# Optimization experiments

Measured on AMD Instinct MI355X. Metric: run time of the kernel, lower is better.

The kernel has to match this reference:

```python
import jax, jax.numpy as jnp
import numpy as np

N = 100000   # nodes
E = 1600000  # edges
H = 64       # hidden_dim
NT = 512     # num_taxo
TD = 32      # taxo_dim
ID = 32      # item_dim
L = 2        # taxo_layers
ETA = 0.5
SLOPE = 0.01  # leaky_relu default


def setup_inputs() -> dict:
    key = jax.random.key(0)
    ks = jax.random.split(key, 20)
    p = lambda i, shape, s: jax.random.normal(ks[i], shape, dtype=jnp.float32) * s
    return {
        'h': p(0, (N, H), 1.0),
        'src': jax.random.randint(ks[1], (E,), 0, N),
        'dst': jax.random.randint(ks[2], (E,), 0, N),
        'taxo_cats': jax.random.randint(ks[3], (N, L), 0, NT),
        'idx_rows': jnp.arange(N),
        'idx_cols': jax.random.randint(ks[4], (N,), 0, N),
        'idx_vals': jax.random.uniform(ks[5], (N,), dtype=jnp.float32),
        'norm_rows': jnp.arange(N),
        'norm_cols': jax.random.randint(ks[6], (N,), 0, N),
        'norm_vals': jax.random.uniform(ks[7], (N,), dtype=jnp.float32),
        'W_w': p(8, (H, H), H ** -0.5),
        'W_b': jnp.zeros((H,), jnp.float32),
        'prelu_a': jnp.full((1,), 0.25, jnp.float32),
        'taxo_mean': p(9, (NT, H), 0.1),
        'taxo_std_log': p(10, (NT, H), 0.1),
        'conv_wh': p(11, (1, 2 * H), (2 * H) ** -0.5),
        'conv_Ww': p(12, (H, H), H ** -0.5),
        'conv_Wb': jnp.zeros((H,), jnp.float32),
        'psi_W': p(13, (1, H, H), H ** -0.5),
        'psi_b': jnp.zeros((1,), jnp.float32),
        'mlp_w0': p(14, (TD, H), H ** -0.5),
        'mlp_b0': jnp.zeros((TD,), jnp.float32),
        'mlp_w1': p(15, (TD, H), H ** -0.5),
        'mlp_b1': jnp.zeros((TD,), jnp.float32),
        'mlp_w2': p(16, (ID, H), H ** -0.5),
        'mlp_b2': jnp.zeros((ID,), jnp.float32),
    }


def _spmm(rows, cols, vals, x, nrows):
    # sparse COO [nrows, n] @ dense [n, d]
    return jax.ops.segment_sum(vals[:, None] * x[cols], rows, num_segments=nrows)


def _edge_softmax(scores, dst, n):
    # softmax of edge scores grouped by destination node
    m = jax.ops.segment_max(scores, dst, num_segments=n)
    e = jnp.exp(scores - m[dst])
    s = jax.ops.segment_sum(e, dst, num_segments=n)
    return e / s[dst]


def _prelu(x, a):
    return jnp.where(x >= 0, x, a * x)


def _normalize(x):
    return x / jnp.maximum(jnp.linalg.norm(x, axis=1, keepdims=True), 1e-12)


def _conv(h, tax, src, dst, wh, Ww, Wb):
    hs = h[src]  # [E,H]
    wf = jnp.concatenate([hs, h[dst]], axis=1) @ wh.T  # [E,1]
    wf = jnp.where(wf >= 0, wf, SLOPE * wf)
    alpha_f = _edge_softmax(wf, dst, N)
    wt = jnp.sum(tax[src] * tax[dst], axis=1, keepdims=True)  # [E,1]
    alpha_t = _edge_softmax(wt, dst, N)
    alpha = ETA * alpha_f + (1.0 - ETA) * alpha_t
    z = jax.ops.segment_sum(hs * alpha, dst, num_segments=N)  # u_mul_e + sum
    return z @ Ww.T + Wb


def reference(h, src, dst, taxo_cats, idx_rows, idx_cols, idx_vals,
              norm_rows, norm_cols, norm_vals, W_w, W_b, prelu_a,
              taxo_mean, taxo_std_log, conv_wh, conv_Ww, conv_Wb,
              psi_W, psi_b, mlp_w0, mlp_b0, mlp_w1, mlp_b1, mlp_w2, mlp_b2):
    h = _prelu(h @ W_w.T + W_b, prelu_a)
    means = taxo_mean[taxo_cats]            # [N,L,H]
    stds = jnp.exp(taxo_std_log[taxo_cats])  # [N,L,H]
    tax = _spmm(norm_rows, norm_cols, norm_vals, means.reshape(N, L * H), N)
    # conv layers share the SAME weights (ModuleList([ConvLayer]*num_layer))
    for i in range(2):
        h = _conv(h, tax, src, dst, conv_wh, conv_Ww, conv_Wb)
        if i < 1:
            h = _prelu(h, prelu_a)
    raw = h
    emb_h = _normalize(h @ mlp_w2.T + mlp_b2)
    embs = []
    for i, (w, b) in enumerate([(mlp_w0, mlp_b0), (mlp_w1, mlp_b1)]):
        h_rev = _spmm(idx_rows, idx_cols, idx_vals, h, N)
        mi = means[:, i]
        si = stds[:, i]
        stpl = jnp.einsum('bi,ij,bj->b', h_rev, psi_W[0], mi)[:, None] + psi_b
        tau = jax.nn.sigmoid(stpl) * jnp.exp(-si)
        cur = (1.0 - tau) * h_rev + tau * mi
        cur = _spmm(norm_rows, norm_cols, norm_vals, cur, N)
        embs.append(_normalize(cur @ w.T + b))
    emb = jnp.stack(embs, axis=2).reshape(N, -1)
    emb = jnp.concatenate([emb_h, emb], axis=1)  # [N, out_dim]
    return raw, emb
```

## Files before the change

### kernel.cpp

```cpp
#include <hip/hip_runtime.h>

constexpr int H  = 64;
constexpr int NT = 512;
constexpr int NBMAX = 512;

#define FMA4(acc_, s_, v_) { (acc_).x += (s_)*(v_).x; (acc_).y += (s_)*(v_).y; \
                             (acc_).z += (s_)*(v_).z; (acc_).w += (s_)*(v_).w; }

__global__ void k_gram(const float* __restrict__ tm, float* __restrict__ G) {
    int idx = blockIdx.x * blockDim.x + threadIdx.x;
    if (idx >= NT * NT) return;
    int a = idx >> 9, b = idx & (NT - 1);
    const float* ra = tm + a * H;
    const float* rb = tm + b * H;
    float s = 0.f;
#pragma unroll
    for (int k = 0; k < H; ++k) s += ra[k] * rb[k];
    G[idx] = s;
}

__global__ void k_nm(const int* __restrict__ ncols, const int* __restrict__ cats,
                     const float* __restrict__ nvals, uint2* __restrict__ nm, int N) {
    int n = blockIdx.x * blockDim.x + threadIdx.x;
    if (n >= N) return;
    int j = ncols[n];
    nm[n] = make_uint2(__float_as_uint(nvals[n]),
                       (unsigned)(cats[j * 2] | (cats[j * 2 + 1] << 16)));
}

__global__ void k_phist(const int* __restrict__ dst, int* __restrict__ histT,
                        int NB, int NPB, int CH, int E) {
    __shared__ int hist[NBMAX];
    int b = blockIdx.x, t = threadIdx.x;
    for (int i = t; i < NB; i += 256) hist[i] = 0;
    __syncthreads();
    int e0 = b * CH, e1 = min(E, e0 + CH);
    for (int e = e0 + t; e < e1; e += 256)
        atomicAdd(&hist[dst[e] >> 8], 1);
    __syncthreads();
    for (int i = t; i < NB; i += 256) histT[i * NPB + b] = hist[i];
}

__global__ void k_btot(const int* __restrict__ histT, int* __restrict__ tot, int NPB) {
    __shared__ int sh[256];
    int bk = blockIdx.x, t = threadIdx.x;
    int s = 0;
    for (int j = t; j < NPB; j += 256) s += histT[bk * NPB + j];
    sh[t] = s;
    __syncthreads();
    for (int o = 128; o; o >>= 1) { if (t < o) sh[t] += sh[t + o]; __syncthreads(); }
    if (!t) tot[bk] = sh[0];
}

__global__ void k_bscan(const int* __restrict__ tot, int* __restrict__ bbase,
                        int* __restrict__ row_start, int NB, int N, int E) {
    __shared__ int sh[NBMAX];
    int t = threadIdx.x;
    int v = (t < NB) ? tot[t] : 0;
    sh[t] = v;
    __syncthreads();
    for (int o = 1; o < NBMAX; o <<= 1) {
        int x = (t >= o) ? sh[t - o] : 0;
        __syncthreads();
        sh[t] += x;
        __syncthreads();
    }
    if (t < NB) bbase[t] = sh[t] - v;
    if (t == 0) { bbase[NB] = E; row_start[N] = E; }
}

__global__ void k_boff(const int* __restrict__ histT, const int* __restrict__ bbase,
                       int* __restrict__ boff, int NPB) {
    __shared__ int sh[NBMAX];
    int bk = blockIdx.x, t = threadIdx.x;
    int v = (t < NPB) ? histT[bk * NPB + t] : 0;
    sh[t] = v;
    __syncthreads();
    for (int o = 1; o < NBMAX; o <<= 1) {
        int x = (t >= o) ? sh[t - o] : 0;
        __syncthreads();
        sh[t] += x;
        __syncthreads();
    }
    if (t < NPB) boff[bk * NPB + t] = bbase[bk] + sh[t] - v;
}

__global__ void k_part(const int* __restrict__ src, const int* __restrict__ dst,
                       const int* __restrict__ boff, unsigned* __restrict__ brec,
                       int NB, int NPB, int CH, int E) {
    __shared__ int cur[NBMAX];
    int b = blockIdx.x, t = threadIdx.x;
    for (int i = t; i < NB; i += 256) cur[i] = boff[i * NPB + b];
    __syncthreads();
    int e0 = b * CH, e1 = min(E, e0 + CH);
    for (int e = e0 + t; e < e1; e += 256) {
        int s = src[e], d = dst[e];
        int pos = atomicAdd(&cur[d >> 8], 1);
        brec[pos] = (unsigned)s | ((unsigned)(d & 255) << 24);
    }
}

__global__ void k_csr(const unsigned* __restrict__ brec, const int* __restrict__ bbase,
                      const uint2* __restrict__ nm, const float* __restrict__ G,
                      int* __restrict__ row_start, int* __restrict__ src_s,
                      float* __restrict__ et, float* __restrict__ sumt, int N) {
    __shared__ int   sdeg[256];
    __shared__ int   scur[256];
    __shared__ float ssum[256];
    __shared__ float snv[256];
    __shared__ int   scc[256];
    int b = blockIdx.x, t = threadIdx.x;
    int node0 = b << 8;
    int ebase = bbase[b], eend = bbase[b + 1];
    sdeg[t] = 0; scur[t] = 0; ssum[t] = 0.f;
    int n = node0 + t;
    if (n < N) { uint2 m = nm[n]; snv[t] = __uint_as_float(m.x); scc[t] = (int)m.y; }
    __syncthreads();
    for (int i = ebase + t; i < eend; i += 256)
        atomicAdd(&sdeg[brec[i] >> 24], 1);
    __syncthreads();
    int val = sdeg[t];
    for (int o = 1; o < 256; o <<= 1) {
        int x = (t >= o) ? sdeg[t - o] : 0;
        __syncthreads();
        sdeg[t] += x;
        __syncthreads();
    }
    int gstart = ebase + sdeg[t] - val;
    if (n < N) row_start[n] = gstart;
    sdeg[t] = gstart;
    __syncthreads();
    for (int i = ebase + t; i < eend; i += 256) {
        unsigned r = brec[i];
        int s = (int)(r & 0xFFFFFFu);
        int j = (int)(r >> 24);
        int c = atomicAdd(&scur[j], 1);
        int k = sdeg[j] + c;
        src_s[k] = s;
        uint2 ms = nm[s];
        float nvs = __uint_as_float(ms.x);
        int cs = (int)ms.y;
        int cd = scc[j];
        float wt = nvs * snv[j] *
                   (G[(cs & 0xffff) * NT + (cd & 0xffff)] + G[(cs >> 16) * NT + (cd >> 16)]);
        float ev = __expf(wt);
        et[k] = ev;
        atomicAdd(&ssum[j], ev);
    }
    __syncthreads();
    if (n < N) sumt[n] = ssum[t];
}

__global__ void k_agg(const float* __restrict__ h_in, const int* __restrict__ src_s,
                      const int* __restrict__ row_start, const float* __restrict__ et,
                      const float* __restrict__ sumt, const float* __restrict__ s_u,
                      const float* __restrict__ s_v, float* __restrict__ z_out, int N) {
    int t = threadIdx.x;
    int sg = t >> 4, l16 = t & 15, f = l16 * 4;
    int n = blockIdx.x * 16 + sg;
    if (n >= N) return;
    int kb = row_start[n], ke = row_start[n + 1];
    float4 z = make_float4(0.f, 0.f, 0.f, 0.f);
    if (ke > kb) {
        float sv = s_v[n];
        float invt = 0.5f / sumt[n];
        float ssf = 0.f;
        float4 zf0 = z, zf1 = z, zt0 = z, zt1 = z;
        for (int k0 = kb; k0 < ke; k0 += 16) {
            int cnt = ke - k0; cnt = cnt < 16 ? cnt : 16;
            int cl = cnt - 1;
            int myk = k0 + (l16 <= cl ? l16 : cl);
            int ms = src_s[myk];
            float me = et[myk] * invt;
            float mw = s_u[ms] + sv;
            mw = mw >= 0.f ? mw : 0.01f * mw;
            float mf = __expf(mw);
            if (l16 > cl) { mf = 0.f; me = 0.f; }
            ssf += mf;
            for (int j0 = 0; j0 < cnt; j0 += 4) {
                int jB = min(j0 + 1, cl), jC = min(j0 + 2, cl), jD = min(j0 + 3, cl);
                int sA = __shfl(ms, j0, 16), sB = __shfl(ms, jB, 16);
                int sC = __shfl(ms, jC, 16), sD = __shfl(ms, jD, 16);
                float tfA = __shfl(mf, j0, 16), tfB = __shfl(mf, jB, 16);
                float tfC = __shfl(mf, jC, 16), tfD = __shfl(mf, jD, 16);
                float teA = __shfl(me, j0, 16), teB = __shfl(me, jB, 16);
                float teC = __shfl(me, jC, 16), teD = __shfl(me, jD, 16);
                float fB = (j0 + 1 <= cl) ? tfB : 0.f;
                float fC = (j0 + 2 <= cl) ? tfC : 0.f;
                float fD = (j0 + 3 <= cl) ? tfD : 0.f;
                float eB = (j0 + 1 <= cl) ? teB : 0.f;
                float eC = (j0 + 2 <= cl) ? teC : 0.f;
                float eD = (j0 + 3 <= cl) ? teD : 0.f;
                const float4 hA = *reinterpret_cast<const float4*>(h_in + (size_t)sA * H + f);
                const float4 hB = *reinterpret_cast<const float4*>(h_in + (size_t)sB * H + f);
                const float4 hC = *reinterpret_cast<const float4*>(h_in + (size_t)sC * H + f);
                const float4 hD = *reinterpret_cast<const float4*>(h_in + (size_t)sD * H + f);
                FMA4(zf0, tfA, hA); FMA4(zt0, teA, hA);
                FMA4(zf1, fB, hB);  FMA4(zt1, eB, hB);
                FMA4(zf0, fC, hC);  FMA4(zt0, eC, hC);
                FMA4(zf1, fD, hD);  FMA4(zt1, eD, hD);
            }
        }
        ssf += __shfl_xor(ssf, 1); ssf += __shfl_xor(ssf, 2);
        ssf += __shfl_xor(ssf, 4); ssf += __shfl_xor(ssf, 8);
        float invf = 0.5f / ssf;
        z.x = (zf0.x + zf1.x) * invf + (zt0.x + zt1.x);
        z.y = (zf0.y + zf1.y) * invf + (zt0.y + zt1.y);
        z.z = (zf0.z + zf1.z) * invf + (zt0.z + zt1.z);
        z.w = (zf0.w + zf1.w) * invf + (zt0.w + zt1.w);
    }
    *reinterpret_cast<float4*>(z_out + (size_t)n * H + f) = z;
}

template <bool PRELU, bool SUV, bool EMBH>
__global__ void __launch_bounds__(256, 4)
k_trans(const float* __restrict__ in, const float* __restrict__ W,
        const float* __restrict__ b, const float* __restrict__ a_ptr,
        const float* __restrict__ wh,
        float* __restrict__ s_u_o, float* __restrict__ s_v_o,
        const float* __restrict__ w2, const float* __restrict__ b2,
        float* __restrict__ emb_out,
        float* __restrict__ out, int N) {
    __shared__ float WF[64 * 68];
    __shared__ float W2T[EMBH ? 64 * 36 : 1];
    __shared__ float xs[4][8][68];
    int t = threadIdx.x;
    for (int i = t; i < 64 * 64; i += 256) { int j = i >> 6, l = i & 63; WF[l * 68 + j] = W[i]; }
    if constexpr (EMBH) {
        for (int i = t; i < 64 * 32; i += 256) { int j = i >> 6, l = i & 63; W2T[l * 36 + j] = w2[i]; }
    }
    __syncthreads();
    int wid = t >> 6, lane = t & 63;
    int g = lane >> 4, f = lane & 15;
    float a = PRELU ? a_ptr[0] : 0.f;
    float4 bias = *reinterpret_cast<const float4*>(b + 4 * f);
    int n0 = blockIdx.x * 32 + wid * 8 + g;
    int n1 = n0 + 4;
    float4 xv0 = make_float4(0.f, 0.f, 0.f, 0.f), xv1 = xv0;
    if (n0 < N) xv0 = *reinterpret_cast<const float4*>(in + (size_t)n0 * H + 4 * f);
    if (n1 < N) xv1 = *reinterpret_cast<const float4*>(in + (size_t)n1 * H + 4 * f);
    *reinterpret_cast<float4*>(&xs[wid][g][4 * f])     = xv0;
    *reinterpret_cast<float4*>(&xs[wid][4 + g][4 * f]) = xv1;
    float4 accP = make_float4(0.f, 0.f, 0.f, 0.f), accQ = accP;
#pragma unroll 2
    for (int l0 = 0; l0 < 64; l0 += 4) {
        const float* wp = &WF[l0 * 68 + 4 * f];
        float4 wv0 = *reinterpret_cast<const float4*>(wp);
        float4 wv1 = *reinterpret_cast<const float4*>(wp + 68);
        float4 wv2 = *reinterpret_cast<const float4*>(wp + 136);
        float4 wv3 = *reinterpret_cast<const float4*>(wp + 204);
        float4 xP = *reinterpret_cast<const float4*>(&xs[wid][g][l0]);
        float4 xQ = *reinterpret_cast<const float4*>(&xs[wid][4 + g][l0]);
        FMA4(accP, xP.x, wv0); FMA4(accP, xP.y, wv1);
        FMA4(accP, xP.z, wv2); FMA4(accP, xP.w, wv3);
        FMA4(accQ, xQ.x, wv0); FMA4(accQ, xQ.y, wv1);
        FMA4(accQ, xQ.z, wv2); FMA4(accQ, xQ.w, wv3);
    }
    auto epi = [&](float4 acc, int n, int slot) {
        acc.x += bias.x; acc.y += bias.y; acc.z += bias.z; acc.w += bias.w;
        if constexpr (PRELU) {
            acc.x = acc.x >= 0.f ? acc.x : a * acc.x;
            acc.y = acc.y >= 0.f ? acc.y : a * acc.y;
            acc.z = acc.z >= 0.f ? acc.z : a * acc.z;
            acc.w = acc.w >= 0.f ? acc.w : a * acc.w;
        }
        if (n < N) *reinterpret_cast<float4*>(out + (size_t)n * H + 4 * f) = acc;
        if constexpr (SUV) {
            float4 wu = *reinterpret_cast<const float4*>(wh + 4 * f);
            float4 wv = *reinterpret_cast<const float4*>(wh + H + 4 * f);
            float u = acc.x * wu.x + acc.y * wu.y + acc.z * wu.z + acc.w * wu.w;
            float v = acc.x * wv.x + acc.y * wv.y + acc.z * wv.z + acc.w * wv.w;
            u += __shfl_xor(u, 1); v += __shfl_xor(v, 1);
            u += __shfl_xor(u, 2); v += __shfl_xor(v, 2);
            u += __shfl_xor(u, 4); v += __shfl_xor(v, 4);
            u += __shfl_xor(u, 8); v += __shfl_xor(v, 8);
            if (f == 0 && n < N) { s_u_o[n] = u; s_v_o[n] = v; }
        }
        if constexpr (EMBH) {
            *reinterpret_cast<float4*>(&xs[wid][slot][4 * f]) = acc;
            if (f < 8) {
                float4 e4 = *reinterpret_cast<const float4*>(b2 + 4 * f);
#pragma unroll 4
                for (int l0 = 0; l0 < 64; l0 += 4) {
                    float4 x4 = *reinterpret_cast<const float4*>(&xs[wid][slot][l0]);
                    float4 u0 = *reinterpret_cast<const float4*>(&W2T[(l0 + 0) * 36 + 4 * f]);
                    float4 u1 = *reinterpret_cast<const float4*>(&W2T[(l0 + 1) * 36 + 4 * f]);
                    float4 u2 = *reinterpret_cast<const float4*>(&W2T[(l0 + 2) * 36 + 4 * f]);
                    float4 u3 = *reinterpret_cast<const float4*>(&W2T[(l0 + 3) * 36 + 4 * f]);
                    FMA4(e4, x4.x, u0); FMA4(e4, x4.y, u1);
                    FMA4(e4, x4.z, u2); FMA4(e4, x4.w, u3);
                }
                float sq = e4.x * e4.x + e4.y * e4.y + e4.z * e4.z + e4.w * e4.w;
                sq += __shfl_xor(sq, 1);
                sq += __shfl_xor(sq, 2);
                sq += __shfl_xor(sq, 4);
                float invn = 1.f / fmaxf(sqrtf(sq), 1e-12f);
                e4.x *= invn; e4.y *= invn; e4.z *= invn; e4.w *= invn;
                if (n < N) *reinterpret_cast<float4*>(emb_out + (size_t)n * 96 + 4 * f) = e4;
            }
        }
    };
    epi(accP, n0, g);
    epi(accQ, n1, 4 + g);
}

__global__ void __launch_bounds__(256, 4)
k_post1(const float* __restrict__ raw, const int* __restrict__ icols,
        const float* __restrict__ ivals, const float* __restrict__ Psi,
        const float* __restrict__ psib, const int* __restrict__ cats,
        const float* __restrict__ tm, const float* __restrict__ tsl,
        float* __restrict__ cur0, float* __restrict__ cur1, int N) {
    __shared__ float PF[64 * 68];
    __shared__ float xs[4][8][68];
    int t = threadIdx.x;
    for (int i = t; i < 64 * 64; i += 256) { int l = i >> 6, j = i & 63; PF[l * 68 + j] = Psi[i]; }
    __syncthreads();
    int wid = t >> 6, lane = t & 63;
    int g = lane >> 4, f = lane & 15;
    float pb = psib[0];
    int n0 = blockIdx.x * 32 + wid * 8 + g;
    int n1 = n0 + 4;
    float4 hr0 = make_float4(0.f, 0.f, 0.f, 0.f), hr1 = hr0;
    if (n0 < N) {
        int c = icols[n0]; float iv = ivals[n0];
        float4 rv = *reinterpret_cast<const float4*>(raw + (size_t)c * H + 4 * f);
        hr0.x = iv * rv.x; hr0.y = iv * rv.y; hr0.z = iv * rv.z; hr0.w = iv * rv.w;
    }
    if (n1 < N) {
        int c = icols[n1]; float iv = ivals[n1];
        float4 rv = *reinterpret_cast<const float4*>(raw + (size_t)c * H + 4 * f);
        hr1.x = iv * rv.x; hr1.y = iv * rv.y; hr1.z = iv * rv.z; hr1.w = iv * rv.w;
    }
    *reinterpret_cast<float4*>(&xs[wid][g][4 * f])     = hr0;
    *reinterpret_cast<float4*>(&xs[wid][4 + g][4 * f]) = hr1;
    float4 v0 = make_float4(0.f, 0.f, 0.f, 0.f), v1 = v0;
#pragma unroll 2
    for (int l0 = 0; l0 < 64; l0 += 4) {
        const float* pp = &PF[l0 * 68 + 4 * f];
        float4 pv0 = *reinterpret_cast<const float4*>(pp);
        float4 pv1 = *reinterpret_cast<const float4*>(pp + 68);
        float4 pv2 = *reinterpret_cast<const float4*>(pp + 136);
        float4 pv3 = *reinterpret_cast<const float4*>(pp + 204);
        float4 xP = *reinterpret_cast<const float4*>(&xs[wid][g][l0]);
        float4 xQ = *reinterpret_cast<const float4*>(&xs[wid][4 + g][l0]);
        FMA4(v0, xP.x, pv0); FMA4(v0, xP.y, pv1); FMA4(v0, xP.z, pv2); FMA4(v0, xP.w, pv3);
        FMA4(v1, xQ.x, pv0); FMA4(v1, xQ.y, pv1); FMA4(v1, xQ.z, pv2); FMA4(v1, xQ.w, pv3);
    }
    auto epi = [&](float4 v, float4 hr, int n) {
        if (n >= N) return;
#pragma unroll
        for (int i2 = 0; i2 < 2; ++i2) {
            int c = cats[n * 2 + i2];
            float4 m4 = *reinterpret_cast<const float4*>(tm + (size_t)c * H + 4 * f);
            float sd = v.x * m4.x + v.y * m4.y + v.z * m4.z + v.w * m4.w;
            sd += __shfl_xor(sd, 1);
            sd += __shfl_xor(sd, 2);
            sd += __shfl_xor(sd, 4);
            sd += __shfl_xor(sd, 8);
            float sig = 1.f / (1.f + __expf(-(sd + pb)));
            float4 t4 = *reinterpret_cast<const float4*>(tsl + (size_t)c * H + 4 * f);
            float4 tau, cv;
            tau.x = sig * __expf(-__expf(t4.x));
            tau.y = sig * __expf(-__expf(t4.y));
            tau.z = sig * __expf(-__expf(t4.z));
            tau.w = sig * __expf(-__expf(t4.w));
            cv.x = (1.f - tau.x) * hr.x + tau.x * m4.x;
            cv.y = (1.f - tau.y) * hr.y + tau.y * m4.y;
            cv.z = (1.f - tau.z) * hr.z + tau.z * m4.z;
            cv.w = (1.f - tau.w) * hr.w + tau.w * m4.w;
            *reinterpret_cast<float4*>((i2 ? cur1 : cur0) + (size_t)n * H + 4 * f) = cv;
        }
    };
    epi(v0, hr0, n0);
    epi(v1, hr1, n1);
}

__global__ void __launch_bounds__(256, 4)
k_post2(const float* __restrict__ cur0, const float* __restrict__ cur1,
        const int* __restrict__ ncols, const float* __restrict__ nvals,
        const float* __restrict__ w0, const float* __restrict__ b0,
        const float* __restrict__ w1, const float* __restrict__ b1,
        float* __restrict__ emb_out, int N) {
    __shared__ float WC[64 * 68];
    __shared__ float xs[4][4][2][68];
    int t = threadIdx.x;
    for (int i = t; i < 64 * 64; i += 256) {
        int j = i >> 6, l = i & 63;
        WC[l * 68 + j] = (j < 32) ? w0[j * 64 + l] : w1[(j - 32) * 64 + l];
    }
    __syncthreads();
    int wid = t >> 6, lane = t & 63;
    int g = lane >> 4, f = lane & 15;
    int half = f >> 3;
    const float* bb = half ? b1 : b0;
    float4 bias = *reinterpret_cast<const float4*>(bb + 4 * (f & 7));
    for (int it = 0; it < 2; ++it) {
        int n = blockIdx.x * 32 + wid * 8 + it * 4 + g;
        float4 x0 = make_float4(0.f, 0.f, 0.f, 0.f), x1 = x0;
        if (n < N) {
            int c = ncols[n];
            float gsc = nvals[n];
            float4 c0v = *reinterpret_cast<const float4*>(cur0 + (size_t)c * H + 4 * f);
            float4 c1v = *reinterpret_cast<const float4*>(cur1 + (size_t)c * H + 4 * f);
            x0.x = gsc * c0v.x; x0.y = gsc * c0v.y; x0.z = gsc * c0v.z; x0.w = gsc * c0v.w;
            x1.x = gsc * c1v.x; x1.y = gsc * c1v.y; x1.z = gsc * c1v.z; x1.w = gsc * c1v.w;
        }
        *reinterpret_cast<float4*>(&xs[wid][g][0][4 * f]) = x0;
        *reinterpret_cast<float4*>(&xs[wid][g][1][4 * f]) = x1;
        float4 acc = bias;
#pragma unroll 4
        for (int l0 = 0; l0 < 64; l0 += 4) {
            float4 x4  = *reinterpret_cast<const float4*>(&xs[wid][g][half][l0]);
            float4 wv0 = *reinterpret_cast<const float4*>(&WC[(l0 + 0) * 68 + 4 * f]);
            float4 wv1 = *reinterpret_cast<const float4*>(&WC[(l0 + 1) * 68 + 4 * f]);
            float4 wv2 = *reinterpret_cast<const float4*>(&WC[(l0 + 2) * 68 + 4 * f]);
            float4 wv3 = *reinterpret_cast<const float4*>(&WC[(l0 + 3) * 68 + 4 * f]);
            FMA4(acc, x4.x, wv0); FMA4(acc, x4.y, wv1);
            FMA4(acc, x4.z, wv2); FMA4(acc, x4.w, wv3);
        }
        float sq = acc.x * acc.x + acc.y * acc.y + acc.z * acc.z + acc.w * acc.w;
        sq += __shfl_xor(sq, 1);
        sq += __shfl_xor(sq, 2);
        sq += __shfl_xor(sq, 4);
        float invn = 1.f / fmaxf(sqrtf(sq), 1e-12f);
        if (n < N) {
            int jb = (f & 7) * 4;
            float* o = emb_out + (size_t)n * 96 + 32 + half;
            o[2 * (jb + 0)] = acc.x * invn;
            o[2 * (jb + 1)] = acc.y * invn;
            o[2 * (jb + 2)] = acc.z * invn;
            o[2 * (jb + 3)] = acc.w * invn;
        }
    }
}

extern "C" void kernel_launch(void* const* d_in, const int* in_sizes, int n_in,
                              void* d_out, int out_size, void* d_ws, size_t ws_size,
                              hipStream_t stream) {
    const float* h      = (const float*)d_in[0];
    const int*   src    = (const int*)d_in[1];
    const int*   dst    = (const int*)d_in[2];
    const int*   cats   = (const int*)d_in[3];
    const int*   icols  = (const int*)d_in[5];
    const float* ivals  = (const float*)d_in[6];
    const int*   ncols  = (const int*)d_in[8];
    const float* nvals  = (const float*)d_in[9];
    const float* W_w    = (const float*)d_in[10];
    const float* W_b    = (const float*)d_in[11];
    const float* pre_a  = (const float*)d_in[12];
    const float* tm     = (const float*)d_in[13];
    const float* tsl    = (const float*)d_in[14];
    const float* wh     = (const float*)d_in[15];
    const float* cWw    = (const float*)d_in[16];
    const float* cWb    = (const float*)d_in[17];
    const float* psiW   = (const float*)d_in[18];
    const float* psib   = (const float*)d_in[19];
    const float* w0     = (const float*)d_in[20];
    const float* b0     = (const float*)d_in[21];
    const float* w1     = (const float*)d_in[22];
    const float* b1     = (const float*)d_in[23];
    const float* w2     = (const float*)d_in[24];
    const float* b2     = (const float*)d_in[25];

    const int N = in_sizes[0] / H;
    const int E = in_sizes[1];
    const int NB = (N + 255) >> 8;
    const int NPB = NB;
    const int CH = (E + NPB - 1) / NPB;

    char* ws = (char*)d_ws;
    size_t off = 0;
    auto alloc = [&](size_t bytes) -> void* {
        void* p = ws + off;
        off = (off + bytes + 255) & ~(size_t)255;
        return p;
    };
    float*    A        = (float*)   alloc((size_t)N * H * 4);
    float*    B        = (float*)   alloc((size_t)N * H * 4);
    float*    Z        = (float*)   alloc((size_t)N * H * 4);
    float*    et       = (float*)   alloc((size_t)E * 4);
    int*      src_s    = (int*)     alloc((size_t)E * 4);
    unsigned* brec     = (unsigned*)alloc((size_t)E * 4);
    uint2*    nm       = (uint2*)   alloc((size_t)N * 8);
    int*      row_start= (int*)     alloc((size_t)(N + 1) * 4);
    float*    sumt     = (float*)   alloc((size_t)N * 4);
    float*    s_u0     = (float*)   alloc((size_t)N * 4);
    float*    s_v0     = (float*)   alloc((size_t)N * 4);
    float*    s_u1     = (float*)   alloc((size_t)N * 4);
    float*    s_v1     = (float*)   alloc((size_t)N * 4);
    float*    G        = (float*)   alloc((size_t)NT * NT * 4);
    int*      histT    = (int*)     alloc((size_t)NB * NPB * 4);
    int*      boff     = (int*)     alloc((size_t)NB * NPB * 4);
    int*      tot      = (int*)     alloc((size_t)NB * 4);
    int*      bbase    = (int*)     alloc((size_t)(NB + 1) * 4);
    (void)ws_size; (void)n_in; (void)out_size;

    float* rawOut  = (float*)d_out;
    float* emb_out = (float*)d_out + (size_t)N * H;

    dim3 b256(256);
    int nb16 = (N + 15) / 16;
    int nb32 = (N + 31) / 32;

    k_gram<<<(NT * NT + 255) / 256, b256, 0, stream>>>(tm, G);
    k_nm<<<(N + 255) / 256, b256, 0, stream>>>(ncols, cats, nvals, nm, N);
    k_phist<<<NPB, b256, 0, stream>>>(dst, histT, NB, NPB, CH, E);
    k_btot<<<NB, b256, 0, stream>>>(histT, tot, NPB);
    k_bscan<<<1, NBMAX, 0, stream>>>(tot, bbase, row_start, NB, N, E);
    k_boff<<<NB, NBMAX, 0, stream>>>(histT, bbase, boff, NPB);
    k_part<<<NPB, b256, 0, stream>>>(src, dst, boff, brec, NB, NPB, CH, E);
    k_csr<<<NB, b256, 0, stream>>>(brec, bbase, nm, G, row_start, src_s, et, sumt, N);

    k_trans<true, true, false><<<nb32, b256, 0, stream>>>(
        h, W_w, W_b, pre_a, wh, s_u0, s_v0, nullptr, nullptr, nullptr, A, N);

    k_agg<<<nb16, b256, 0, stream>>>(A, src_s, row_start, et, sumt, s_u0, s_v0, Z, N);
    k_trans<true, true, false><<<nb32, b256, 0, stream>>>(
        Z, cWw, cWb, pre_a, wh, s_u1, s_v1, nullptr, nullptr, nullptr, B, N);

    k_agg<<<nb16, b256, 0, stream>>>(B, src_s, row_start, et, sumt, s_u1, s_v1, Z, N);
    k_trans<false, false, true><<<nb32, b256, 0, stream>>>(
        Z, cWw, cWb, pre_a, nullptr, nullptr, nullptr, w2, b2, emb_out, rawOut, N);

    k_post1<<<nb32, b256, 0, stream>>>(rawOut, icols, ivals, psiW, psib, cats, tm, tsl,
                                       A, B, N);
    k_post2<<<nb32, b256, 0, stream>>>(A, B, ncols, nvals, w0, b0, w1, b1, emb_out, N);
}
```

Before: 354.8 us.

## Fuse edge aggregation with the dense transform, and fold k_nm into k_phist

Aggregation and the following 64x64 transform (with PReLU, attention-score projection, or the emb_h head) now run in one kernel, k_aggt, via a small per-group staging buffer in shared memory. This removes the round trip of the intermediate Z array through global memory and two kernel launches. Each 16-node block now loads the full weight matrix into shared memory, which adds per-block setup and shared-memory pressure. The node-metadata pack (k_nm) is merged into the histogram kernel, which assumes the histogram grid has at least N/256 blocks.

```diff
diff --git a/kernel.cpp b/kernel.cpp
--- a/kernel.cpp
+++ b/kernel.cpp
@@ -19,19 +19,18 @@
     G[idx] = s;
 }
 
-__global__ void k_nm(const int* __restrict__ ncols, const int* __restrict__ cats,
-                     const float* __restrict__ nvals, uint2* __restrict__ nm, int N) {
-    int n = blockIdx.x * blockDim.x + threadIdx.x;
-    if (n >= N) return;
-    int j = ncols[n];
-    nm[n] = make_uint2(__float_as_uint(nvals[n]),
-                       (unsigned)(cats[j * 2] | (cats[j * 2 + 1] << 16)));
-}
-
 __global__ void k_phist(const int* __restrict__ dst, int* __restrict__ histT,
-                        int NB, int NPB, int CH, int E) {
+                        const int* __restrict__ ncols, const int* __restrict__ cats,
+                        const float* __restrict__ nvals, uint2* __restrict__ nm,
+                        int NB, int NPB, int CH, int E, int N) {
     __shared__ int hist[NBMAX];
     int b = blockIdx.x, t = threadIdx.x;
+    int gid = b * 256 + t;
+    if (gid < N) {
+        int j = ncols[gid];
+        nm[gid] = make_uint2(__float_as_uint(nvals[gid]),
+                             (unsigned)(cats[j * 2] | (cats[j * 2 + 1] << 16)));
+    }
     for (int i = t; i < NB; i += 256) hist[i] = 0;
     __syncthreads();
     int e0 = b * CH, e1 = min(E, e0 + CH);
@@ -151,65 +150,139 @@
     if (n < N) sumt[n] = ssum[t];
 }
 
-__global__ void k_agg(const float* __restrict__ h_in, const int* __restrict__ src_s,
-                      const int* __restrict__ row_start, const float* __restrict__ et,
-                      const float* __restrict__ sumt, const float* __restrict__ s_u,
-                      const float* __restrict__ s_v, float* __restrict__ z_out, int N) {
+#define LDH(S) (*reinterpret_cast<const float4*>(h_in + (size_t)(S) * H + f))
+template <bool PRELU, bool SUV, bool EMBH>
+__global__ void k_aggt(const float* __restrict__ h_in, const int* __restrict__ src_s,
+                       const int* __restrict__ row_start, const float* __restrict__ et,
+                       const float* __restrict__ sumt, const float* __restrict__ s_u,
+                       const float* __restrict__ s_v,
+                       const float* __restrict__ W, const float* __restrict__ b,
+                       const float* __restrict__ a_ptr, const float* __restrict__ wh,
+                       float* __restrict__ s_u_o, float* __restrict__ s_v_o,
+                       const float* __restrict__ w2, const float* __restrict__ b2,
+                       float* __restrict__ emb_out,
+                       float* __restrict__ out, int N) {
+    __shared__ float WF[64 * 68];
+    __shared__ float W2T[EMBH ? 64 * 36 : 1];
+    __shared__ float xs[4][4][68];
     int t = threadIdx.x;
+    for (int i = t; i < 64 * 64; i += 256) { int j = i >> 6, l = i & 63; WF[l * 68 + j] = W[i]; }
+    if constexpr (EMBH) {
+        for (int i = t; i < 64 * 32; i += 256) { int j = i >> 6, l = i & 63; W2T[l * 36 + j] = w2[i]; }
+    }
+    __syncthreads();
     int sg = t >> 4, l16 = t & 15, f = l16 * 4;
+    int wid = t >> 6, g = sg & 3;
     int n = blockIdx.x * 16 + sg;
-    if (n >= N) return;
-    int kb = row_start[n], ke = row_start[n + 1];
+
     float4 z = make_float4(0.f, 0.f, 0.f, 0.f);
-    if (ke > kb) {
-        float sv = s_v[n];
-        float invt = 0.5f / sumt[n];
-        float ssf = 0.f;
-        float4 zf0 = z, zf1 = z, zt0 = z, zt1 = z;
-        for (int k0 = kb; k0 < ke; k0 += 16) {
-            int cnt = ke - k0; cnt = cnt < 16 ? cnt : 16;
-            int cl = cnt - 1;
-            int myk = k0 + (l16 <= cl ? l16 : cl);
-            int ms = src_s[myk];
-            float me = et[myk] * invt;
-            float mw = s_u[ms] + sv;
-            mw = mw >= 0.f ? mw : 0.01f * mw;
-            float mf = __expf(mw);
-            if (l16 > cl) { mf = 0.f; me = 0.f; }
-            ssf += mf;
-            for (int j0 = 0; j0 < cnt; j0 += 4) {
-                int jB = min(j0 + 1, cl), jC = min(j0 + 2, cl), jD = min(j0 + 3, cl);
-                int sA = __shfl(ms, j0, 16), sB = __shfl(ms, jB, 16);
-                int sC = __shfl(ms, jC, 16), sD = __shfl(ms, jD, 16);
-                float tfA = __shfl(mf, j0, 16), tfB = __shfl(mf, jB, 16);
-                float tfC = __shfl(mf, jC, 16), tfD = __shfl(mf, jD, 16);
-                float teA = __shfl(me, j0, 16), teB = __shfl(me, jB, 16);
-                float teC = __shfl(me, jC, 16), teD = __shfl(me, jD, 16);
-                float fB = (j0 + 1 <= cl) ? tfB : 0.f;
-                float fC = (j0 + 2 <= cl) ? tfC : 0.f;
-                float fD = (j0 + 3 <= cl) ? tfD : 0.f;
-                float eB = (j0 + 1 <= cl) ? teB : 0.f;
-                float eC = (j0 + 2 <= cl) ? teC : 0.f;
-                float eD = (j0 + 3 <= cl) ? teD : 0.f;
-                const float4 hA = *reinterpret_cast<const float4*>(h_in + (size_t)sA * H + f);
-                const float4 hB = *reinterpret_cast<const float4*>(h_in + (size_t)sB * H + f);
-                const float4 hC = *reinterpret_cast<const float4*>(h_in + (size_t)sC * H + f);
-                const float4 hD = *reinterpret_cast<const float4*>(h_in + (size_t)sD * H + f);
-                FMA4(zf0, tfA, hA); FMA4(zt0, teA, hA);
-                FMA4(zf1, fB, hB);  FMA4(zt1, eB, hB);
-                FMA4(zf0, fC, hC);  FMA4(zt0, eC, hC);
-                FMA4(zf1, fD, hD);  FMA4(zt1, eD, hD);
+    if (n < N) {
+        int kb = row_start[n], ke = row_start[n + 1];
+        if (ke > kb) {
+            float sv = s_v[n];
+            float invt = 0.5f / sumt[n];
+            float ssf = 0.f;
+            float4 zf0 = z, zf1 = z, zt0 = z, zt1 = z;
+            for (int k0 = kb; k0 < ke; k0 += 16) {
+                int cnt = ke - k0; cnt = cnt < 16 ? cnt : 16;
+                int cl = cnt - 1;
+                int myk = k0 + (l16 <= cl ? l16 : cl);
+                int ms = src_s[myk];
+                float me = et[myk] * invt;
+                float mw = s_u[ms] + sv;
+                mw = mw >= 0.f ? mw : 0.01f * mw;
+                float mf = __expf(mw);
+                if (l16 > cl) { mf = 0.f; me = 0.f; }
+                ssf += mf;
+                for (int j0 = 0; j0 < cnt; j0 += 4) {
+                    int jB = min(j0 + 1, cl), jC = min(j0 + 2, cl), jD = min(j0 + 3, cl);
+                    int sA = __shfl(ms, j0, 16), sB = __shfl(ms, jB, 16);
+                    int sC = __shfl(ms, jC, 16), sD = __shfl(ms, jD, 16);
+                    float tfA = __shfl(mf, j0, 16), tfB = __shfl(mf, jB, 16);
+                    float tfC = __shfl(mf, jC, 16), tfD = __shfl(mf, jD, 16);
+                    float teA = __shfl(me, j0, 16), teB = __shfl(me, jB, 16);
+                    float teC = __shfl(me, jC, 16), teD = __shfl(me, jD, 16);
+                    float fB = (j0 + 1 <= cl) ? tfB : 0.f;
+                    float fC = (j0 + 2 <= cl) ? tfC : 0.f;
+                    float fD = (j0 + 3 <= cl) ? tfD : 0.f;
+                    float eB = (j0 + 1 <= cl) ? teB : 0.f;
+                    float eC = (j0 + 2 <= cl) ? teC : 0.f;
+                    float eD = (j0 + 3 <= cl) ? teD : 0.f;
+                    const float4 hA = LDH(sA);
+                    const float4 hB = LDH(sB);
+                    const float4 hC = LDH(sC);
+                    const float4 hD = LDH(sD);
+                    FMA4(zf0, tfA, hA); FMA4(zt0, teA, hA);
+                    FMA4(zf1, fB, hB);  FMA4(zt1, eB, hB);
+                    FMA4(zf0, fC, hC);  FMA4(zt0, eC, hC);
+                    FMA4(zf1, fD, hD);  FMA4(zt1, eD, hD);
+                }
             }
-        }
-        ssf += __shfl_xor(ssf, 1); ssf += __shfl_xor(ssf, 2);
-        ssf += __shfl_xor(ssf, 4); ssf += __shfl_xor(ssf, 8);
-        float invf = 0.5f / ssf;
-        z.x = (zf0.x + zf1.x) * invf + (zt0.x + zt1.x);
-        z.y = (zf0.y + zf1.y) * invf + (zt0.y + zt1.y);
-        z.z = (zf0.z + zf1.z) * invf + (zt0.z + zt1.z);
-        z.w = (zf0.w + zf1.w) * invf + (zt0.w + zt1.w);
-    }
-    *reinterpret_cast<float4*>(z_out + (size_t)n * H + f) = z;
+            ssf += __shfl_xor(ssf, 1); ssf += __shfl_xor(ssf, 2);
+            ssf += __shfl_xor(ssf, 4); ssf += __shfl_xor(ssf, 8);
+            float invf = 0.5f / ssf;
+            z.x = (zf0.x + zf1.x) * invf + (zt0.x + zt1.x);
+            z.y = (zf0.y + zf1.y) * invf + (zt0.y + zt1.y);
+            z.z = (zf0.z + zf1.z) * invf + (zt0.z + zt1.z);
+            z.w = (zf0.w + zf1.w) * invf + (zt0.w + zt1.w);
+        }
+    }
+
+    *reinterpret_cast<float4*>(&xs[wid][g][f]) = z;
+    float a = PRELU ? a_ptr[0] : 0.f;
+    float4 acc = *reinterpret_cast<const float4*>(b + f);
+#pragma unroll 2
+    for (int l0 = 0; l0 < 64; l0 += 4) {
+        const float* wp = &WF[l0 * 68 + f];
+        float4 wv0 = *reinterpret_cast<const float4*>(wp);
+        float4 wv1 = *reinterpret_cast<const float4*>(wp + 68);
+        float4 wv2 = *reinterpret_cast<const float4*>(wp + 136);
+        float4 wv3 = *reinterpret_cast<const float4*>(wp + 204);
+        float4 x4 = *reinterpret_cast<const float4*>(&xs[wid][g][l0]);
+        FMA4(acc, x4.x, wv0); FMA4(acc, x4.y, wv1);
+        FMA4(acc, x4.z, wv2); FMA4(acc, x4.w, wv3);
+    }
+    if constexpr (PRELU) {
+        acc.x = acc.x >= 0.f ? acc.x : a * acc.x;
+        acc.y = acc.y >= 0.f ? acc.y : a * acc.y;
+        acc.z = acc.z >= 0.f ? acc.z : a * acc.z;
+        acc.w = acc.w >= 0.f ? acc.w : a * acc.w;
+    }
+    if (n < N) *reinterpret_cast<float4*>(out + (size_t)n * H + f) = acc;
+    if constexpr (SUV) {
+        float4 wu = *reinterpret_cast<const float4*>(wh + f);
+        float4 wv = *reinterpret_cast<const float4*>(wh + H + f);
+        float u = acc.x * wu.x + acc.y * wu.y + acc.z * wu.z + acc.w * wu.w;
+        float v = acc.x * wv.x + acc.y * wv.y + acc.z * wv.z + acc.w * wv.w;
+        u += __shfl_xor(u, 1); v += __shfl_xor(v, 1);
+        u += __shfl_xor(u, 2); v += __shfl_xor(v, 2);
+        u += __shfl_xor(u, 4); v += __shfl_xor(v, 4);
+        u += __shfl_xor(u, 8); v += __shfl_xor(v, 8);
+        if (l16 == 0 && n < N) { s_u_o[n] = u; s_v_o[n] = v; }
+    }
+    if constexpr (EMBH) {
+        *reinterpret_cast<float4*>(&xs[wid][g][f]) = acc;
+        if (l16 < 8) {
+            float4 e4 = *reinterpret_cast<const float4*>(b2 + f);
+#pragma unroll 4
+            for (int l0 = 0; l0 < 64; l0 += 4) {
+                float4 x4 = *reinterpret_cast<const float4*>(&xs[wid][g][l0]);
+                float4 u0 = *reinterpret_cast<const float4*>(&W2T[(l0 + 0) * 36 + f]);
+                float4 u1 = *reinterpret_cast<const float4*>(&W2T[(l0 + 1) * 36 + f]);
+                float4 u2 = *reinterpret_cast<const float4*>(&W2T[(l0 + 2) * 36 + f]);
+                float4 u3 = *reinterpret_cast<const float4*>(&W2T[(l0 + 3) * 36 + f]);
+                FMA4(e4, x4.x, u0); FMA4(e4, x4.y, u1);
+                FMA4(e4, x4.z, u2); FMA4(e4, x4.w, u3);
+            }
+            float sq = e4.x * e4.x + e4.y * e4.y + e4.z * e4.z + e4.w * e4.w;
+            sq += __shfl_xor(sq, 1);
+            sq += __shfl_xor(sq, 2);
+            sq += __shfl_xor(sq, 4);
+            float invn = 1.f / fmaxf(sqrtf(sq), 1e-12f);
+            e4.x *= invn; e4.y *= invn; e4.z *= invn; e4.w *= invn;
+            if (n < N) *reinterpret_cast<float4*>(emb_out + (size_t)n * 96 + f) = e4;
+        }
+    }
 }
 
 template <bool PRELU, bool SUV, bool EMBH>
@@ -493,7 +566,7 @@
     int*      boff     = (int*)     alloc((size_t)NB * NPB * 4);
     int*      tot      = (int*)     alloc((size_t)NB * 4);
     int*      bbase    = (int*)     alloc((size_t)(NB + 1) * 4);
-    (void)ws_size; (void)n_in; (void)out_size;
+    (void)ws_size; (void)n_in; (void)out_size; (void)Z;
 
     float* rawOut  = (float*)d_out;
     float* emb_out = (float*)d_out + (size_t)N * H;
@@ -503,8 +576,8 @@
     int nb32 = (N + 31) / 32;
 
     k_gram<<<(NT * NT + 255) / 256, b256, 0, stream>>>(tm, G);
-    k_nm<<<(N + 255) / 256, b256, 0, stream>>>(ncols, cats, nvals, nm, N);
-    k_phist<<<NPB, b256, 0, stream>>>(dst, histT, NB, NPB, CH, E);
+    k_phist<<<NPB, b256, 0, stream>>>(dst, histT, ncols, cats, nvals, nm,
+                                      NB, NPB, CH, E, N);
     k_btot<<<NB, b256, 0, stream>>>(histT, tot, NPB);
     k_bscan<<<1, NBMAX, 0, stream>>>(tot, bbase, row_start, NB, N, E);
     k_boff<<<NB, NBMAX, 0, stream>>>(histT, bbase, boff, NPB);
@@ -514,13 +587,13 @@
     k_trans<true, true, false><<<nb32, b256, 0, stream>>>(
         h, W_w, W_b, pre_a, wh, s_u0, s_v0, nullptr, nullptr, nullptr, A, N);
 
-    k_agg<<<nb16, b256, 0, stream>>>(A, src_s, row_start, et, sumt, s_u0, s_v0, Z, N);
-    k_trans<true, true, false><<<nb32, b256, 0, stream>>>(
-        Z, cWw, cWb, pre_a, wh, s_u1, s_v1, nullptr, nullptr, nullptr, B, N);
-
-    k_agg<<<nb16, b256, 0, stream>>>(B, src_s, row_start, et, sumt, s_u1, s_v1, Z, N);
-    k_trans<false, false, true><<<nb32, b256, 0, stream>>>(
-        Z, cWw, cWb, pre_a, nullptr, nullptr, nullptr, w2, b2, emb_out, rawOut, N);
+    k_aggt<true, true, false><<<nb16, b256, 0, stream>>>(
+        A, src_s, row_start, et, sumt, s_u0, s_v0,
+        cWw, cWb, pre_a, wh, s_u1, s_v1, nullptr, nullptr, nullptr, B, N);
+
+    k_aggt<false, false, true><<<nb16, b256, 0, stream>>>(
+        B, src_s, row_start, et, sumt, s_u1, s_v1,
+        cWw, cWb, pre_a, nullptr, nullptr, nullptr, w2, b2, emb_out, rawOut, N);
 
     k_post1<<<nb32, b256, 0, stream>>>(rawOut, icols, ivals, psiW, psib, cats, tm, tsl,
                                        A, B, N);
```

Result: faster. 329.3 us (-7.2%).
